# Kernel tuning notes

Hardware: AMD Instinct MI355X
Metric: run time of the kernel (lower is better)

The kernel has to match this reference:

```python
import jax, jax.numpy as jnp
import numpy as np
import math

B, S, D, H = 4, 2048, 1024, 16
DK = D // H


def setup_inputs() -> dict:
    key = jax.random.key(0)
    ks = jax.random.split(key, 12)
    scale = 1.0 / math.sqrt(D)
    inp = {
        "x": jax.random.normal(ks[0], (B, S, D), jnp.float32),
        "q": jax.random.normal(ks[1], (B, S, D), jnp.float32),
        "k": jax.random.normal(ks[2], (B, S, D), jnp.float32),
        "v": jax.random.normal(ks[3], (B, S, D), jnp.float32),
        # causal mask: 1 = keep, 0 = masked
        "mask": jnp.tril(jnp.ones((S, S), jnp.int32))[None, None],
        "wq": jax.random.normal(ks[4], (D, D), jnp.float32) * scale,
        "bq": jnp.zeros((D,), jnp.float32),
        "wk": jax.random.normal(ks[5], (D, D), jnp.float32) * scale,
        "bk": jnp.zeros((D,), jnp.float32),
        "wv": jax.random.normal(ks[6], (D, D), jnp.float32) * scale,
        "bv": jnp.zeros((D,), jnp.float32),
        "wo": jax.random.normal(ks[7], (D, D), jnp.float32) * scale,
        "bo": jnp.zeros((D,), jnp.float32),
    }
    return inp


def _split_heads(t):  # [B,S,D] -> [B,H,S,DK]
    return t.reshape(B, S, H, DK).transpose(0, 2, 1, 3)


def reference(x, q, k, v, mask, wq, bq, wk, bk, wv, bv, wo, bo):
    # x is accepted for signature parity with the torch module but is
    # overwritten inside the original forward; it does not affect output.
    query = _split_heads(q @ wq + bq)
    key_h = _split_heads(k @ wk + bk)
    value = _split_heads(v @ wv + bv)
    # scores: [B,H,Sq,Sk]
    scores = jnp.einsum("bhqd,bhkd->bhqk", query, key_h) / math.sqrt(DK)
    scores = jnp.where(mask == 0, jnp.float32(-1e9), scores)
    attn = jax.nn.softmax(scores, axis=-1)  # dropout p=0.0 -> identity
    out = jnp.einsum("bhqk,bhkd->bhqd", attn, value)
    out = out.transpose(0, 2, 1, 3).reshape(B, S, D)
    return out @ wo + bo
```

## Files before the change

kernel.cpp:

```cpp
#include <hip/hip_runtime.h>

typedef unsigned short u16;
typedef __bf16 bf16x8 __attribute__((ext_vector_type(8)));
typedef float f32x4 __attribute__((ext_vector_type(4)));
typedef u16 u16x8 __attribute__((ext_vector_type(8)));
typedef u16 u16x4 __attribute__((ext_vector_type(4)));

static constexpr int Bb = 4, Ss = 2048, Dd = 1024, Hh = 16, DKk = 64;
static constexpr int Mg = Bb * Ss;
static constexpr int Kg = Dd;
static constexpr int Ng = Dd;

#if __has_builtin(__builtin_amdgcn_exp2f)
#define EXP2 __builtin_amdgcn_exp2f
#else
#define EXP2 exp2f
#endif

__device__ __forceinline__ u16 f2b(float f) {
    union { __bf16 h; u16 u; } c; c.h = (__bf16)f; return c.u;
}

typedef const __attribute__((address_space(1))) void gas_t;
typedef __attribute__((address_space(3))) void las_t;
__device__ __forceinline__ void gll16(const void* g, void* l) {
    __builtin_amdgcn_global_load_lds((gas_t*)g, (las_t*)l, 16, 0, 0);
}

__global__ __launch_bounds__(256) void conv3_kernel(const float* __restrict__ q,
                                                    const float* __restrict__ k,
                                                    const float* __restrict__ v,
                                                    u16* __restrict__ dst) {
    const size_t per = (size_t)Mg * Kg / 8;
    size_t id = (size_t)blockIdx.x * 256 + threadIdx.x;
    size_t t = id / per, off = (id % per) * 8;
    const float* src = (t == 0) ? q : (t == 1) ? k : v;
    float4 a = *(const float4*)(src + off);
    float4 b = *(const float4*)(src + off + 4);
    u16x8 o;
    o[0] = f2b(a.x); o[1] = f2b(a.y); o[2] = f2b(a.z); o[3] = f2b(a.w);
    o[4] = f2b(b.x); o[5] = f2b(b.y); o[6] = f2b(b.z); o[7] = f2b(b.w);
    *(u16x8*)(dst + t * (size_t)Mg * Kg + off) = o;
}

__global__ __launch_bounds__(256) void wt4_kernel(const float* w0, const float* w1,
                                                  const float* w2, const float* w3,
                                                  u16* t0, u16* t1, u16* t2, u16* t3) {
    const float* W; u16* Wt;
    switch (blockIdx.z) {
        case 0: W = w0; Wt = t0; break;
        case 1: W = w1; Wt = t1; break;
        case 2: W = w2; Wt = t2; break;
        default: W = w3; Wt = t3; break;
    }
    __shared__ __attribute__((aligned(16))) u16 T[64 * 72];
    const int k0 = blockIdx.x * 64, n0 = blockIdx.y * 64;
    const int tid = threadIdx.x;
    for (int i = 0; i < 4; ++i) {
        int flat = tid + i * 256;
        int r = flat >> 4, c4 = flat & 15;
        float4 w4 = *(const float4*)(W + (size_t)(k0 + r) * 1024 + n0 + c4 * 4);
        u16* d = &T[r * 72 + c4 * 4];
        d[0] = f2b(w4.x); d[1] = f2b(w4.y); d[2] = f2b(w4.z); d[3] = f2b(w4.w);
    }
    __syncthreads();
    for (int i = 0; i < 2; ++i) {
        int flat = tid + i * 256;
        int n = flat >> 3, c8 = flat & 7;
        u16x8 v;
        for (int jj = 0; jj < 8; ++jj) v[jj] = T[(c8 * 8 + jj) * 72 + n];
        *(u16x8*)(Wt + (size_t)(n0 + n) * 1024 + k0 + c8 * 8) = v;
    }
}

__global__ __launch_bounds__(256) void qkv_gemm(
    const u16* __restrict__ Ac,
    const u16* __restrict__ WqT, const u16* __restrict__ WkT,
    const u16* __restrict__ WvT,
    const float* __restrict__ bq, const float* __restrict__ bk,
    const float* __restrict__ bv,
    u16* __restrict__ Qw, u16* __restrict__ Kw, u16* __restrict__ VwT,
    float qscale) {
    __shared__ __attribute__((aligned(16))) u16 As[128 * 32];
    __shared__ __attribute__((aligned(16))) u16 Bs[128 * 32];
    const int z = blockIdx.z;
    const u16* A = Ac + (size_t)z * Mg * Kg;
    const u16* Bt = (z == 0) ? WqT : (z == 1) ? WkT : WvT;
    const float* bias = (z == 0) ? bq : (z == 1) ? bk : bv;
    const float scale = (z == 0) ? qscale : 1.0f;

    const int tid = threadIdx.x;
    const int wave = tid >> 6, lane = tid & 63;
    const int quad = lane >> 4, l15 = lane & 15;
    const int m0 = blockIdx.x * 128, n0 = blockIdx.y * 128;
    const int wm = (wave >> 1) * 64, wn = (wave & 1) * 64;
    const int rr = lane >> 2, cc = (lane & 3) * 8;

    const u16* Ag = A + (size_t)(m0 + wave * 32 + rr) * Kg + cc;
    const u16* Bg = Bt + (size_t)(n0 + wave * 32 + rr) * Kg + cc;
    u16* Asw = &As[wave * 32 * 32];
    u16* Bsw = &Bs[wave * 32 * 32];

    f32x4 acc[4][4] = {};

    for (int k0 = 0; k0 < Kg; k0 += 32) {
        __syncthreads();
        gll16(Ag + k0, Asw);
        gll16(Ag + k0 + (size_t)16 * Kg, Asw + 16 * 32);
        gll16(Bg + k0, Bsw);
        gll16(Bg + k0 + (size_t)16 * Kg, Bsw + 16 * 32);
        __syncthreads();

        bf16x8 a[4], b[4];
        for (int i = 0; i < 4; ++i)
            a[i] = *(const bf16x8*)(&As[(wm + i * 16 + l15) * 32 + quad * 8]);
        for (int j = 0; j < 4; ++j)
            b[j] = *(const bf16x8*)(&Bs[(wn + j * 16 + l15) * 32 + quad * 8]);
        if (z < 2) {
            for (int i = 0; i < 4; ++i)
                for (int j = 0; j < 4; ++j)
                    acc[i][j] = __builtin_amdgcn_mfma_f32_16x16x32_bf16(b[j], a[i], acc[i][j], 0, 0, 0);
        } else {
            for (int i = 0; i < 4; ++i)
                for (int j = 0; j < 4; ++j)
                    acc[i][j] = __builtin_amdgcn_mfma_f32_16x16x32_bf16(a[i], b[j], acc[i][j], 0, 0, 0);
        }
    }

    if (z < 2) {
        u16* Out = (z == 0) ? Qw : Kw;
        for (int i = 0; i < 4; ++i) {
            int m_row = m0 + wm + i * 16 + l15;
            int bb = m_row >> 11, s = m_row & 2047;
            for (int j = 0; j < 4; ++j) {
                int nb = n0 + wn + j * 16 + quad * 4;
                float4 b4 = *(const float4*)(bias + nb);
                int h = nb >> 6, dk = nb & 63;
                u16x4 pk;
                pk[0] = f2b((acc[i][j][0] + b4.x) * scale);
                pk[1] = f2b((acc[i][j][1] + b4.y) * scale);
                pk[2] = f2b((acc[i][j][2] + b4.z) * scale);
                pk[3] = f2b((acc[i][j][3] + b4.w) * scale);
                *(u16x4*)(Out + (((size_t)bb * Hh + h) * Ss + s) * DKk + dk) = pk;
            }
        }
    } else {
        for (int i = 0; i < 4; ++i) {
            for (int j = 0; j < 4; ++j) {
                int col = n0 + wn + j * 16 + l15;
                float bvv = bias[col];
                int h = col >> 6, dk = col & 63;
                int row0 = m0 + wm + i * 16 + quad * 4;
                int bb = row0 >> 11, s0 = row0 & 2047;
                u16x4 pk;
                for (int r = 0; r < 4; ++r) pk[r] = f2b(acc[i][j][r] + bvv);
                *(u16x4*)(VwT + (((size_t)bb * Hh + h) * DKk + dk) * Ss + s0) = pk;
            }
        }
    }
}

__global__ __launch_bounds__(256) void out_gemm(const u16* __restrict__ A,
                                                const u16* __restrict__ Bt,
                                                const float* __restrict__ bias,
                                                float* __restrict__ Out) {
    __shared__ __attribute__((aligned(16))) u16 As[128 * 32];
    __shared__ __attribute__((aligned(16))) u16 Bs[128 * 32];
    const int tid = threadIdx.x;
    const int wave = tid >> 6, lane = tid & 63;
    const int quad = lane >> 4, l15 = lane & 15;
    const int m0 = blockIdx.x * 128, n0 = blockIdx.y * 128;
    const int wm = (wave >> 1) * 64, wn = (wave & 1) * 64;
    const int rr = lane >> 2, cc = (lane & 3) * 8;

    const u16* Ag = A + (size_t)(m0 + wave * 32 + rr) * Kg + cc;
    const u16* Bg = Bt + (size_t)(n0 + wave * 32 + rr) * Kg + cc;
    u16* Asw = &As[wave * 32 * 32];
    u16* Bsw = &Bs[wave * 32 * 32];

    f32x4 acc[4][4] = {};

    for (int k0 = 0; k0 < Kg; k0 += 32) {
        __syncthreads();
        gll16(Ag + k0, Asw);
        gll16(Ag + k0 + (size_t)16 * Kg, Asw + 16 * 32);
        gll16(Bg + k0, Bsw);
        gll16(Bg + k0 + (size_t)16 * Kg, Bsw + 16 * 32);
        __syncthreads();

        bf16x8 a[4], b[4];
        for (int i = 0; i < 4; ++i)
            a[i] = *(const bf16x8*)(&As[(wm + i * 16 + l15) * 32 + quad * 8]);
        for (int j = 0; j < 4; ++j)
            b[j] = *(const bf16x8*)(&Bs[(wn + j * 16 + l15) * 32 + quad * 8]);
        for (int i = 0; i < 4; ++i)
            for (int j = 0; j < 4; ++j)
                acc[i][j] = __builtin_amdgcn_mfma_f32_16x16x32_bf16(b[j], a[i], acc[i][j], 0, 0, 0);
    }

    for (int i = 0; i < 4; ++i) {
        int m_row = m0 + wm + i * 16 + l15;
        for (int j = 0; j < 4; ++j) {
            int nb = n0 + wn + j * 16 + quad * 4;
            float4 b4 = *(const float4*)(bias + nb);
            float4 o;
            o.x = acc[i][j][0] + b4.x;
            o.y = acc[i][j][1] + b4.y;
            o.z = acc[i][j][2] + b4.z;
            o.w = acc[i][j][3] + b4.w;
            *(float4*)(Out + (size_t)m_row * Ng + nb) = o;
        }
    }
}

__global__ __launch_bounds__(256) void attn_kernel(const u16* __restrict__ Qw,
                                                   const u16* __restrict__ Kw,
                                                   const u16* __restrict__ Vt,
                                                   u16* __restrict__ Ow) {
    __shared__ __attribute__((aligned(16))) u16 QPs[4608];
    __shared__ __attribute__((aligned(16))) u16 Ks[4096];
    __shared__ __attribute__((aligned(16))) u16 Vs[4096];

    const int idx = blockIdx.x;
    const int qt = (Ss / 64 - 1) - (idx >> 6);
    const int bh = idx & 63;
    const int q0 = qt * 64;
    const int tid = threadIdx.x, wave = tid >> 6, lane = tid & 63;
    const int quad = lane >> 4, l15 = lane & 15;
    const int rr = lane >> 2, cc = (lane & 3) * 8;

    const u16* Qb = Qw + (size_t)bh * Ss * DKk;
    const u16* Kb = Kw + (size_t)bh * Ss * DKk;
    const u16* Vb = Vt + (size_t)bh * DKk * Ss;

    for (int kc = 0; kc < 2; ++kc)
        gll16(Qb + (size_t)(q0 + wave * 16 + rr) * DKk + kc * 32 + cc,
              &QPs[kc * 2048 + wave * 16 * 32]);
    __syncthreads();
    bf16x8 aq0 = *(const bf16x8*)(&QPs[(wave * 16 + l15) * 32 + quad * 8]);
    bf16x8 aq1 = *(const bf16x8*)(&QPs[2048 + (wave * 16 + l15) * 32 + quad * 8]);

    f32x4 acc_o[4] = {};
    float l_r = 0.f;
    const int qrow = q0 + wave * 16 + l15;
    u16* Pw = &QPs[wave * 1152];

    for (int j = 0; j <= qt; ++j) {
        __syncthreads();
        for (int c = 0; c < 2; ++c) {
            gll16(Kb + (size_t)(j * 64 + wave * 16 + rr) * DKk + c * 32 + cc,
                  &Ks[c * 2048 + wave * 16 * 32]);
            gll16(Vb + (size_t)(wave * 16 + rr) * Ss + j * 64 + c * 32 + cc,
                  &Vs[c * 2048 + wave * 16 * 32]);
        }
        __syncthreads();

        f32x4 sacc[4];
        for (int ct = 0; ct < 4; ++ct) {
            bf16x8 bk0 = *(const bf16x8*)(&Ks[(ct * 16 + l15) * 32 + quad * 8]);
            bf16x8 bk1 = *(const bf16x8*)(&Ks[2048 + (ct * 16 + l15) * 32 + quad * 8]);
            f32x4 z = {};
            z = __builtin_amdgcn_mfma_f32_16x16x32_bf16(bk0, aq0, z, 0, 0, 0);
            z = __builtin_amdgcn_mfma_f32_16x16x32_bf16(bk1, aq1, z, 0, 0, 0);
            sacc[ct] = z;
        }

        if (j == qt) {
            for (int ct = 0; ct < 4; ++ct) {
                int kbase = j * 64 + ct * 16 + quad * 4;
                for (int r = 0; r < 4; ++r)
                    if (kbase + r > qrow) sacc[ct][r] = -1e30f;
            }
        }

        const float M0 = 8.0f;
        float sum = 0.f;
        for (int ct = 0; ct < 4; ++ct)
            for (int r = 0; r < 4; ++r) {
                float p = EXP2(sacc[ct][r] - M0);
                sacc[ct][r] = p;
                sum += p;
            }
        l_r += sum;

        for (int ct = 0; ct < 4; ++ct) {
            u16x4 pk;
            for (int r = 0; r < 4; ++r) pk[r] = f2b(sacc[ct][r]);
            *(u16x4*)(&Pw[l15 * 72 + ct * 16 + quad * 4]) = pk;
        }

        for (int sc = 0; sc < 2; ++sc) {
            bf16x8 ap = *(const bf16x8*)(&Pw[l15 * 72 + sc * 32 + quad * 8]);
            for (int dt = 0; dt < 4; ++dt) {
                bf16x8 bv = *(const bf16x8*)(&Vs[sc * 2048 + (dt * 16 + l15) * 32 + quad * 8]);
                acc_o[dt] = __builtin_amdgcn_mfma_f32_16x16x32_bf16(bv, ap, acc_o[dt], 0, 0, 0);
            }
        }
    }

    const int b = bh >> 4, h = bh & 15;
    float L = l_r;
    L += __shfl_xor(L, 16, 64);
    L += __shfl_xor(L, 32, 64);
    const float inv = 1.f / L;
    const int s = q0 + wave * 16 + l15;
    u16* orow = Ow + (((size_t)b * Ss + s) * Hh + h) * DKk;
    for (int dt = 0; dt < 4; ++dt) {
        u16x4 pk;
        for (int r = 0; r < 4; ++r) pk[r] = f2b(acc_o[dt][r] * inv);
        *(u16x4*)(orow + dt * 16 + quad * 4) = pk;
    }
}

extern "C" void kernel_launch(void* const* d_in, const int* in_sizes, int n_in,
                              void* d_out, int out_size, void* d_ws, size_t ws_size,
                              hipStream_t stream) {
    const float* q  = (const float*)d_in[1];
    const float* k  = (const float*)d_in[2];
    const float* v  = (const float*)d_in[3];
    const float* wq = (const float*)d_in[5];
    const float* bq = (const float*)d_in[6];
    const float* wk = (const float*)d_in[7];
    const float* bk = (const float*)d_in[8];
    const float* wv = (const float*)d_in[9];
    const float* bv = (const float*)d_in[10];
    const float* wo = (const float*)d_in[11];
    const float* bo = (const float*)d_in[12];
    float* out = (float*)d_out;

    u16* WqT = (u16*)d_ws;
    u16* WkT = WqT + 1024 * 1024;
    u16* WvT = WkT + 1024 * 1024;
    u16* WoT = WvT + 1024 * 1024;
    u16* Ac  = WoT + 1024 * 1024;
    u16* Qw  = Ac + (size_t)3 * Mg * Kg;
    u16* Kw  = Qw + (size_t)Mg * Kg;
    u16* VwT = Kw + (size_t)Mg * Kg;
    u16* Ow  = Ac;

    conv3_kernel<<<dim3(3 * (Mg * Kg / 8) / 256), 256, 0, stream>>>(q, k, v, Ac);
    wt4_kernel<<<dim3(16, 16, 4), 256, 0, stream>>>(wq, wk, wv, wo, WqT, WkT, WvT, WoT);

    const float qscale = 0.125f * 1.44269504f;
    qkv_gemm<<<dim3(Mg / 128, Ng / 128, 3), 256, 0, stream>>>(
        Ac, WqT, WkT, WvT, bq, bk, bv, Qw, Kw, VwT, qscale);

    attn_kernel<<<dim3(2048), 256, 0, stream>>>(Qw, Kw, VwT, Ow);

    out_gemm<<<dim3(Mg / 128, Ng / 128), 256, 0, stream>>>(Ow, WoT, bo, out);
}
```

Measured before the change: 356.5 us.

## Rewrite QKV GEMM as 256x256 eight-wave double-buffered pipelined kernel

Replaces the 128x128, four-wave QKV projection GEMM with a 256x256 tile kernel of eight waves. It uses K=64 stages, XOR-swizzled LDS layout and double-buffered async global-to-LDS loads interleaved with MFMA phases, plus setprio around the MFMA bursts. The V case swaps the A/B operands so the transposed output keeps the same accumulator mapping. This targets global-load latency stalls, LDS bank conflicts and the low operand reuse of the smaller tile. In exchange it adds many explicit barriers, uses 128KB of LDS, and raises register pressure.

Measured after the change: 349.1 us. -2.1%, faster.

```diff
diff --git a/kernel.cpp b/kernel.cpp
--- a/kernel.cpp
+++ b/kernel.cpp
@@ -26,6 +26,10 @@
 __device__ __forceinline__ void gll16(const void* g, void* l) {
     __builtin_amdgcn_global_load_lds((gas_t*)g, (las_t*)l, 16, 0, 0);
 }
+
+#define BARM  asm volatile("s_barrier" ::: "memory")
+#define LGKM0 asm volatile("s_waitcnt lgkmcnt(0)" ::: "memory")
+#define VMW(n) asm volatile("s_waitcnt vmcnt(" #n ")" ::: "memory")
 
 __global__ __launch_bounds__(256) void conv3_kernel(const float* __restrict__ q,
                                                     const float* __restrict__ k,
@@ -73,22 +77,193 @@
     }
 }
 
-__global__ __launch_bounds__(256) void qkv_gemm(
+static constexpr int TILE = 256 * 64;
+static constexpr int HALF = 128 * 64;
+
+__device__ __forceinline__ void stage_half(const u16* s, u16* dst, int wave,
+                                           int half, int kt) {
+#pragma unroll
+    for (int l = 0; l < 2; ++l) {
+        const int c = wave * 2 + l;
+        gll16(s + (size_t)(half * 128 + c * 8) * Kg + kt * 64, dst + c * 512);
+    }
+}
+
+__device__ __forceinline__ void readA8(const u16* base, int wm, int mh,
+                                       int l15, int quad, bf16x8* a) {
+#pragma unroll
+    for (int i = 0; i < 4; ++i) {
+        const int row = wm * 128 + mh * 64 + i * 16 + l15;
+        const u16* rp = base + row * 64;
+        const int sw = row & 7;
+        a[i * 2]     = *(const bf16x8*)(rp + ((quad)     ^ sw) * 8);
+        a[i * 2 + 1] = *(const bf16x8*)(rp + ((quad + 4) ^ sw) * 8);
+    }
+}
+
+__device__ __forceinline__ void readB4(const u16* base, int wn, int nh,
+                                       int l15, int quad, bf16x8* b) {
+#pragma unroll
+    for (int j = 0; j < 2; ++j) {
+        const int row = wn * 64 + nh * 32 + j * 16 + l15;
+        const u16* rp = base + row * 64;
+        const int sw = row & 7;
+        b[j * 2]     = *(const bf16x8*)(rp + ((quad)     ^ sw) * 8);
+        b[j * 2 + 1] = *(const bf16x8*)(rp + ((quad + 4) ^ sw) * 8);
+    }
+}
+
+__device__ __forceinline__ void mfma16f(f32x4 (&acc)[8][4], int mh, int nh,
+                                        const bf16x8* a, const bf16x8* b) {
+    __builtin_amdgcn_s_setprio(1);
+#pragma unroll
+    for (int i = 0; i < 4; ++i)
+#pragma unroll
+        for (int j = 0; j < 2; ++j) {
+            f32x4 c = acc[mh * 4 + i][nh * 2 + j];
+            c = __builtin_amdgcn_mfma_f32_16x16x32_bf16(b[j * 2],     a[i * 2],     c, 0, 0, 0);
+            c = __builtin_amdgcn_mfma_f32_16x16x32_bf16(b[j * 2 + 1], a[i * 2 + 1], c, 0, 0, 0);
+            acc[mh * 4 + i][nh * 2 + j] = c;
+        }
+    __builtin_amdgcn_s_setprio(0);
+}
+
+__device__ __forceinline__ void gemm256_core(const u16* __restrict__ Asrc,
+                                             const u16* __restrict__ Bsrc,
+                                             u16* As, u16* Bs,
+                                             f32x4 (&acc)[8][4]) {
+    const int tid = threadIdx.x;
+    const int wave = tid >> 6, lane = tid & 63;
+    const int quad = lane >> 4, l15 = lane & 15;
+    const int wm = wave >> 2, wn = wave & 3;
+    const int r0 = lane >> 3, gsw = (lane & 7) ^ r0;
+    const u16* sA = Asrc + (size_t)r0 * Kg + gsw * 8;
+    const u16* sB = Bsrc + (size_t)r0 * Kg + gsw * 8;
+
+    stage_half(sA, As + 0 * TILE + 0 * HALF, wave, 0, 0);
+    stage_half(sA, As + 0 * TILE + 1 * HALF, wave, 1, 0);
+    stage_half(sB, Bs + 0 * TILE + 0 * HALF, wave, 0, 0);
+    stage_half(sB, Bs + 0 * TILE + 1 * HALF, wave, 1, 0);
+    stage_half(sB, Bs + 1 * TILE + 0 * HALF, wave, 0, 1);
+    stage_half(sB, Bs + 1 * TILE + 1 * HALF, wave, 1, 1);
+    VMW(4); BARM;
+
+    bf16x8 aF[8], b0F[4], b1F[4];
+#pragma unroll 1
+    for (int it = 0; it < 8; ++it) {
+        const int t1 = 2 * it + 1;
+        const int s2 = (2 * it + 2) & 15, s3 = (2 * it + 3) & 15;
+        readA8(As + 0 * TILE, wm, 0, l15, quad, aF);
+        readB4(Bs + 0 * TILE, wn, 0, l15, quad, b0F);
+        stage_half(sA, As + 1 * TILE + 0 * HALF, wave, 0, t1);
+        BARM; LGKM0;
+        mfma16f(acc, 0, 0, aF, b0F);
+        BARM;
+        readB4(Bs + 0 * TILE, wn, 1, l15, quad, b1F);
+        stage_half(sA, As + 1 * TILE + 1 * HALF, wave, 1, t1);
+        BARM; LGKM0;
+        mfma16f(acc, 0, 1, aF, b1F);
+        BARM;
+        readA8(As + 0 * TILE, wm, 1, l15, quad, aF);
+        stage_half(sB, Bs + 0 * TILE + 0 * HALF, wave, 0, s2);
+        BARM; LGKM0;
+        mfma16f(acc, 1, 1, aF, b1F);
+        BARM;
+        stage_half(sB, Bs + 0 * TILE + 1 * HALF, wave, 1, s2);
+        mfma16f(acc, 1, 0, aF, b0F);
+        VMW(4); BARM;
+        readA8(As + 1 * TILE, wm, 0, l15, quad, aF);
+        readB4(Bs + 1 * TILE, wn, 0, l15, quad, b0F);
+        stage_half(sA, As + 0 * TILE + 0 * HALF, wave, 0, s2);
+        BARM; LGKM0;
+        mfma16f(acc, 0, 0, aF, b0F);
+        BARM;
+        readB4(Bs + 1 * TILE, wn, 1, l15, quad, b1F);
+        stage_half(sA, As + 0 * TILE + 1 * HALF, wave, 1, s2);
+        BARM; LGKM0;
+        mfma16f(acc, 0, 1, aF, b1F);
+        BARM;
+        readA8(As + 1 * TILE, wm, 1, l15, quad, aF);
+        stage_half(sB, Bs + 1 * TILE + 0 * HALF, wave, 0, s3);
+        BARM; LGKM0;
+        mfma16f(acc, 1, 1, aF, b1F);
+        BARM;
+        stage_half(sB, Bs + 1 * TILE + 1 * HALF, wave, 1, s3);
+        mfma16f(acc, 1, 0, aF, b0F);
+        VMW(4); BARM;
+    }
+    VMW(0);
+}
+
+__global__ __launch_bounds__(512, 2) void qkv_gemm8(
     const u16* __restrict__ Ac,
     const u16* __restrict__ WqT, const u16* __restrict__ WkT,
-    const u16* __restrict__ WvT,
+    const u16* __restrict__ WvTw,
     const float* __restrict__ bq, const float* __restrict__ bk,
     const float* __restrict__ bv,
-    u16* __restrict__ Qw, u16* __restrict__ Kw, u16* __restrict__ VwT,
+    u16* __restrict__ Qw, u16* __restrict__ Kw, u16* __restrict__ Vout,
     float qscale) {
-    __shared__ __attribute__((aligned(16))) u16 As[128 * 32];
-    __shared__ __attribute__((aligned(16))) u16 Bs[128 * 32];
+    __shared__ __attribute__((aligned(16))) u16 As[2 * TILE];
+    __shared__ __attribute__((aligned(16))) u16 Bs[2 * TILE];
     const int z = blockIdx.z;
-    const u16* A = Ac + (size_t)z * Mg * Kg;
-    const u16* Bt = (z == 0) ? WqT : (z == 1) ? WkT : WvT;
-    const float* bias = (z == 0) ? bq : (z == 1) ? bk : bv;
-    const float scale = (z == 0) ? qscale : 1.0f;
-
+    const int m0 = blockIdx.x * 256, n0 = blockIdx.y * 256;
+    const u16* Asrc; const u16* Bsrc; const float* bias;
+    if (z == 0)      { Asrc = Ac + (size_t)m0 * Kg;                    Bsrc = WqT + (size_t)n0 * Kg; bias = bq; }
+    else if (z == 1) { Asrc = Ac + (size_t)Mg * Kg + (size_t)m0 * Kg;  Bsrc = WkT + (size_t)n0 * Kg; bias = bk; }
+    else             { Asrc = WvTw + (size_t)n0 * Kg;                  Bsrc = Ac + (size_t)2 * Mg * Kg + (size_t)m0 * Kg; bias = bv; }
+
+    f32x4 acc[8][4] = {};
+    gemm256_core(Asrc, Bsrc, As, Bs, acc);
+
+    const int tid = threadIdx.x, wave = tid >> 6, lane = tid & 63;
+    const int quad = lane >> 4, l15 = lane & 15;
+    const int wm = wave >> 2, wn = wave & 3;
+
+    if (z < 2) {
+        const float scale = (z == 0) ? qscale : 1.0f;
+        u16* Out = (z == 0) ? Qw : Kw;
+#pragma unroll
+        for (int i = 0; i < 8; ++i) {
+            const int m_row = m0 + wm * 128 + i * 16 + l15;
+            const int bb = m_row >> 11, s = m_row & 2047;
+#pragma unroll
+            for (int j = 0; j < 4; ++j) {
+                const int nb = n0 + wn * 64 + j * 16 + quad * 4;
+                float4 b4 = *(const float4*)(bias + nb);
+                const int h = nb >> 6, dk = nb & 63;
+                u16x4 pk;
+                pk[0] = f2b((acc[i][j][0] + b4.x) * scale);
+                pk[1] = f2b((acc[i][j][1] + b4.y) * scale);
+                pk[2] = f2b((acc[i][j][2] + b4.z) * scale);
+                pk[3] = f2b((acc[i][j][3] + b4.w) * scale);
+                *(u16x4*)(Out + (((size_t)bb * Hh + h) * Ss + s) * DKk + dk) = pk;
+            }
+        }
+    } else {
+#pragma unroll
+        for (int i = 0; i < 8; ++i) {
+            const int n = n0 + wm * 128 + i * 16 + l15;
+            const int h = n >> 6, dk = n & 63;
+            const float bvv = bias[n];
+#pragma unroll
+            for (int j = 0; j < 4; ++j) {
+                const int mq = m0 + wn * 64 + j * 16 + quad * 4;
+                const int bb = mq >> 11, s0 = mq & 2047;
+                u16x4 pk;
+#pragma unroll
+                for (int r = 0; r < 4; ++r) pk[r] = f2b(acc[i][j][r] + bvv);
+                *(u16x4*)(Vout + (((size_t)bb * Hh + h) * DKk + dk) * Ss + s0) = pk;
+            }
+        }
+    }
+}
+
+__global__ __launch_bounds__(256) void out_gemm(const u16* __restrict__ A,
+                                                const u16* __restrict__ Bt,
+                                                const float* __restrict__ bias,
+                                                float* __restrict__ Out) {
+    __shared__ __attribute__((aligned(16))) u16 Asm[128 * 32];
+    __shared__ __attribute__((aligned(16))) u16 Bsm[128 * 32];
     const int tid = threadIdx.x;
     const int wave = tid >> 6, lane = tid & 63;
     const int quad = lane >> 4, l15 = lane & 15;
@@ -98,8 +273,8 @@
 
     const u16* Ag = A + (size_t)(m0 + wave * 32 + rr) * Kg + cc;
     const u16* Bg = Bt + (size_t)(n0 + wave * 32 + rr) * Kg + cc;
-    u16* Asw = &As[wave * 32 * 32];
-    u16* Bsw = &Bs[wave * 32 * 32];
+    u16* Asw = &Asm[wave * 32 * 32];
+    u16* Bsw = &Bsm[wave * 32 * 32];
 
     f32x4 acc[4][4] = {};
 
@@ -113,86 +288,9 @@
 
         bf16x8 a[4], b[4];
         for (int i = 0; i < 4; ++i)
-            a[i] = *(const bf16x8*)(&As[(wm + i * 16 + l15) * 32 + quad * 8]);
+            a[i] = *(const bf16x8*)(&Asm[(wm + i * 16 + l15) * 32 + quad * 8]);
         for (int j = 0; j < 4; ++j)
-            b[j] = *(const bf16x8*)(&Bs[(wn + j * 16 + l15) * 32 + quad * 8]);
-        if (z < 2) {
-            for (int i = 0; i < 4; ++i)
-                for (int j = 0; j < 4; ++j)
-                    acc[i][j] = __builtin_amdgcn_mfma_f32_16x16x32_bf16(b[j], a[i], acc[i][j], 0, 0, 0);
-        } else {
-            for (int i = 0; i < 4; ++i)
-                for (int j = 0; j < 4; ++j)
-                    acc[i][j] = __builtin_amdgcn_mfma_f32_16x16x32_bf16(a[i], b[j], acc[i][j], 0, 0, 0);
-        }
-    }
-
-    if (z < 2) {
-        u16* Out = (z == 0) ? Qw : Kw;
-        for (int i = 0; i < 4; ++i) {
-            int m_row = m0 + wm + i * 16 + l15;
-            int bb = m_row >> 11, s = m_row & 2047;
-            for (int j = 0; j < 4; ++j) {
-                int nb = n0 + wn + j * 16 + quad * 4;
-                float4 b4 = *(const float4*)(bias + nb);
-                int h = nb >> 6, dk = nb & 63;
-                u16x4 pk;
-                pk[0] = f2b((acc[i][j][0] + b4.x) * scale);
-                pk[1] = f2b((acc[i][j][1] + b4.y) * scale);
-                pk[2] = f2b((acc[i][j][2] + b4.z) * scale);
-                pk[3] = f2b((acc[i][j][3] + b4.w) * scale);
-                *(u16x4*)(Out + (((size_t)bb * Hh + h) * Ss + s) * DKk + dk) = pk;
-            }
-        }
-    } else {
-        for (int i = 0; i < 4; ++i) {
-            for (int j = 0; j < 4; ++j) {
-                int col = n0 + wn + j * 16 + l15;
-                float bvv = bias[col];
-                int h = col >> 6, dk = col & 63;
-                int row0 = m0 + wm + i * 16 + quad * 4;
-                int bb = row0 >> 11, s0 = row0 & 2047;
-                u16x4 pk;
-                for (int r = 0; r < 4; ++r) pk[r] = f2b(acc[i][j][r] + bvv);
-                *(u16x4*)(VwT + (((size_t)bb * Hh + h) * DKk + dk) * Ss + s0) = pk;
-            }
-        }
-    }
-}
-
-__global__ __launch_bounds__(256) void out_gemm(const u16* __restrict__ A,
-                                                const u16* __restrict__ Bt,
-                                                const float* __restrict__ bias,
-                                                float* __restrict__ Out) {
-    __shared__ __attribute__((aligned(16))) u16 As[128 * 32];
-    __shared__ __attribute__((aligned(16))) u16 Bs[128 * 32];
-    const int tid = threadIdx.x;
-    const int wave = tid >> 6, lane = tid & 63;
-    const int quad = lane >> 4, l15 = lane & 15;
-    const int m0 = blockIdx.x * 128, n0 = blockIdx.y * 128;
-    const int wm = (wave >> 1) * 64, wn = (wave & 1) * 64;
-    const int rr = lane >> 2, cc = (lane & 3) * 8;
-
-    const u16* Ag = A + (size_t)(m0 + wave * 32 + rr) * Kg + cc;
-    const u16* Bg = Bt + (size_t)(n0 + wave * 32 + rr) * Kg + cc;
-    u16* Asw = &As[wave * 32 * 32];
-    u16* Bsw = &Bs[wave * 32 * 32];
-
-    f32x4 acc[4][4] = {};
-
-    for (int k0 = 0; k0 < Kg; k0 += 32) {
-        __syncthreads();
-        gll16(Ag + k0, Asw);
-        gll16(Ag + k0 + (size_t)16 * Kg, Asw + 16 * 32);
-        gll16(Bg + k0, Bsw);
-        gll16(Bg + k0 + (size_t)16 * Kg, Bsw + 16 * 32);
-        __syncthreads();
-
-        bf16x8 a[4], b[4];
-        for (int i = 0; i < 4; ++i)
-            a[i] = *(const bf16x8*)(&As[(wm + i * 16 + l15) * 32 + quad * 8]);
-        for (int j = 0; j < 4; ++j)
-            b[j] = *(const bf16x8*)(&Bs[(wn + j * 16 + l15) * 32 + quad * 8]);
+            b[j] = *(const bf16x8*)(&Bsm[(wn + j * 16 + l15) * 32 + quad * 8]);
         for (int i = 0; i < 4; ++i)
             for (int j = 0; j < 4; ++j)
                 acc[i][j] = __builtin_amdgcn_mfma_f32_16x16x32_bf16(b[j], a[i], acc[i][j], 0, 0, 0);
@@ -342,7 +440,7 @@
     wt4_kernel<<<dim3(16, 16, 4), 256, 0, stream>>>(wq, wk, wv, wo, WqT, WkT, WvT, WoT);
 
     const float qscale = 0.125f * 1.44269504f;
-    qkv_gemm<<<dim3(Mg / 128, Ng / 128, 3), 256, 0, stream>>>(
+    qkv_gemm8<<<dim3(Mg / 256, Ng / 256, 3), 512, 0, stream>>>(
         Ac, WqT, WkT, WvT, bq, bk, bv, Qw, Kw, VwT, qscale);
 
     attn_kernel<<<dim3(2048), 256, 0, stream>>>(Qw, Kw, VwT, Ow);
```
